# Kernel optimization log

Measured on AMD Instinct MI355X. Metric: run time of the kernel, lower is better.

Reference implementation:

```python
import jax, jax.numpy as jnp
import numpy as np

B, S = 16, 512
VD, TD, H, NH = 768, 768, 1024, 16
HD = H // NH
MAXREL = 128
THRESH = 2.0 / 3.0


def _bitlinear(x, W, b):
    # BitNet b1.58 eval-mode: ternary-quantize weights, rescale, dense matmul
    s = jnp.clip(jnp.mean(jnp.abs(W)), 1e-5, 1000.0)
    wn = jnp.clip(W / s, -10.0, 10.0)
    q = jnp.where(wn > THRESH, 1.0, jnp.where(wn < -THRESH, -1.0, 0.0))
    return x @ (q * s).T + b


def _ln(x, g, b, eps=1e-5):
    m = jnp.mean(x, axis=-1, keepdims=True)
    v = jnp.mean((x - m) ** 2, axis=-1, keepdims=True)
    return (x - m) * jax.lax.rsqrt(v + eps) * g + b


def setup_inputs() -> dict:
    key = jax.random.key(0)
    ks = jax.random.split(key, 10)
    def n(k, shape, std=0.02):
        return jax.random.normal(k, shape, dtype=jnp.float32) * std
    return dict(
        vision_features=jax.random.normal(ks[0], (B, VD), dtype=jnp.float32),
        text_features=jax.random.normal(ks[1], (B, S, TD), dtype=jnp.float32),
        W_vp=n(ks[2], (H, VD)), b_vp=jnp.zeros((H,), jnp.float32),
        W_tp=n(ks[3], (H, TD)), b_tp=jnp.zeros((H,), jnp.float32),
        W_tqkv=n(ks[4], (3 * H, H)), b_tqkv=jnp.zeros((3 * H,), jnp.float32),
        W_vout=n(ks[5], (H, H)), b_vout=jnp.zeros((H,), jnp.float32),
        W_tout=n(ks[6], (H, H)), b_tout=jnp.zeros((H,), jnp.float32),
        g_tn=jnp.ones((H,), jnp.float32), be_tn=jnp.zeros((H,), jnp.float32),
        g_i2t=jnp.ones((H,), jnp.float32), be_i2t=jnp.zeros((H,), jnp.float32),
        g_t2i=jnp.ones((H,), jnp.float32), be_t2i=jnp.zeros((H,), jnp.float32),
        alpha_i2t=jnp.zeros((1,), jnp.float32),
        alpha_t2i=jnp.zeros((1,), jnp.float32),
        rel_embed=n(ks[7], (2 * MAXREL + 1, NH)),
        text_mask=jnp.ones((B, S), dtype=bool),
    )


def reference(vision_features, text_features, W_vp, b_vp, W_tp, b_tp,
              W_tqkv, b_tqkv, W_vout, b_vout, W_tout, b_tout,
              g_tn, be_tn, g_i2t, be_i2t, g_t2i, be_t2i,
              alpha_i2t, alpha_t2i, rel_embed, text_mask):
    scale = HD ** -0.5
    vision_proj = _bitlinear(vision_features, W_vp, b_vp)            # [B,H]
    text_proj = _bitlinear(text_features, W_tp, b_tp)                # [B,S,H]

    # --- text self-attention with relative-position bias ---
    qkv = _bitlinear(_ln(text_proj, g_tn, be_tn), W_tqkv, b_tqkv)    # [B,S,3H]
    qkv = qkv.reshape(B, S, 3, NH, HD).transpose(2, 0, 3, 1, 4)      # [3,B,nh,S,hd]
    q, k, v = qkv[0], qkv[1], qkv[2]
    attn = jnp.einsum('bhqd,bhkd->bhqk', q, k) * scale
    coords = jnp.arange(S)
    rel = jnp.clip(coords[:, None] - coords[None, :], -MAXREL, MAXREL) + MAXREL
    attn = attn + rel_embed[rel].transpose(2, 0, 1)[None]            # +[1,nh,S,S]
    attn = jnp.where(text_mask[:, None, None, :], attn, -1e9)
    attn = jax.nn.softmax(attn, axis=-1)
    text_self = jnp.einsum('bhqk,bhkd->bhqd', attn, v)
    text_self = text_self.transpose(0, 2, 1, 3).reshape(B, S, H)
    text_self = text_proj + text_self                                # residual

    # --- image -> text cross-attention (vision token queries text) ---
    vq = jnp.broadcast_to(vision_proj[:, None], (B, S, H))
    vq = vq.reshape(B, S, NH, HD).transpose(0, 2, 1, 3)              # [B,nh,S,hd]
    tkv = text_self.reshape(B, S, NH, HD).transpose(0, 2, 1, 3)      # [B,nh,S,hd]
    i2t = jnp.einsum('bhqd,bhkd->bhqk', vq, tkv) * scale
    i2t = jnp.where(text_mask[:, None, None, :], i2t, -1e9)
    i2t = jax.nn.softmax(i2t, axis=-1)
    i2t_out = jnp.einsum('bhqk,bhkd->bhqd', i2t, tkv)
    i2t_out = i2t_out.transpose(0, 2, 1, 3).reshape(B, S, H).mean(axis=1)
    i2t_out = _ln(i2t_out, g_i2t, be_i2t)                            # [B,H]
    fused_vision = vision_proj + alpha_i2t * _bitlinear(i2t_out, W_vout, b_vout)

    # --- text -> image cross-attention (text queries single vision token) ---
    tq = text_self.reshape(B, S, NH, HD).transpose(0, 2, 1, 3)       # [B,nh,S,hd]
    vkv = vision_proj.reshape(B, 1, NH, HD).transpose(0, 2, 1, 3)    # [B,nh,1,hd]
    t2i = jnp.einsum('bhqd,bhkd->bhqk', tq, vkv) * scale             # [B,nh,S,1]
    t2i = jax.nn.softmax(t2i, axis=-1)
    t2i_out = jnp.einsum('bhqk,bhkd->bhqd', t2i, vkv)
    t2i_out = t2i_out.transpose(0, 2, 1, 3).reshape(B, S, H)
    t2i_out = _ln(t2i_out, g_t2i, be_t2i)
    fused_text = text_self + alpha_t2i * _bitlinear(t2i_out, W_tout, b_tout)

    return fused_vision, fused_text
```

## Files before the change

### kernel.cpp

```cpp
#include <hip/hip_runtime.h>
#include <cstdint>

#define B_   16
#define S_   512
#define VD_  768
#define TD_  768
#define H_   1024
#define NH_  16
#define HD_  64
#define H3_  3072

typedef __attribute__((ext_vector_type(8))) short bf16x8;
typedef __attribute__((ext_vector_type(4))) float f32x4;

__device__ __forceinline__ float b2f(unsigned short h) {
  union { unsigned u; float f; } x; x.u = ((unsigned)h) << 16; return x.f;
}
__device__ __forceinline__ unsigned short f2b(float f) {
  union { float f; unsigned u; } x; x.f = f;
  unsigned r = x.u + 0x7fffu + ((x.u >> 16) & 1u);
  return (unsigned short)(r >> 16);
}
__device__ __forceinline__ unsigned cvt_pk_bf16(float lo, float hi) {
  unsigned r;
  __asm__("v_cvt_pk_bf16_f32 %0, %1, %2" : "=v"(r) : "v"(lo), "v"(hi));
  return r;
}
__device__ __forceinline__ float fexp2(float x) {
#if __has_builtin(__builtin_amdgcn_exp2f)
  return __builtin_amdgcn_exp2f(x);
#else
  return exp2f(x);
#endif
}

__device__ __forceinline__ void gload_lds16(const void* g, void* lds) {
  __builtin_amdgcn_global_load_lds(
      (const __attribute__((address_space(1))) unsigned int*)g,
      (__attribute__((address_space(3))) unsigned int*)lds, 16, 0, 0);
}
__device__ __forceinline__ void lds_wave_fence() {
  __asm__ __volatile__("s_waitcnt lgkmcnt(0)" ::: "memory");
}

__global__ __launch_bounds__(256) void k_abssum_cvt(const float* __restrict__ w0, int n0,
                                                    const float* __restrict__ w1, int n1,
                                                    const float* __restrict__ w2, int n2,
                                                    const float* __restrict__ w3, int n3,
                                                    const float* __restrict__ w4, int n4,
                                                    double* __restrict__ partials,
                                                    const float* __restrict__ cvt_in,
                                                    unsigned short* __restrict__ cvt_out,
                                                    int cvt_n4) {
  int y = blockIdx.y;
  if (y == 5) {
    for (int i = blockIdx.x * 256 + threadIdx.x; i < cvt_n4; i += 128 * 256) {
      float4 v = ((const float4*)cvt_in)[i];
      ushort4 o; o.x = f2b(v.x); o.y = f2b(v.y); o.z = f2b(v.z); o.w = f2b(v.w);
      ((ushort4*)cvt_out)[i] = o;
    }
    return;
  }
  const float* w = y == 0 ? w0 : y == 1 ? w1 : y == 2 ? w2 : y == 3 ? w3 : w4;
  int n4q = (y == 0 ? n0 : y == 1 ? n1 : y == 2 ? n2 : y == 3 ? n3 : n4) >> 2;
  double s = 0.0;
  for (int i = blockIdx.x * 256 + threadIdx.x; i < n4q; i += 128 * 256) {
    float4 v = ((const float4*)w)[i];
    s += (double)fabsf(v.x) + (double)fabsf(v.y) + (double)fabsf(v.z) + (double)fabsf(v.w);
  }
#pragma unroll
  for (int off = 32; off > 0; off >>= 1) s += __shfl_down(s, off, 64);
  __shared__ double red[4];
  if ((threadIdx.x & 63) == 0) red[threadIdx.x >> 6] = s;
  __syncthreads();
  if (threadIdx.x == 0)
    partials[y * 128 + blockIdx.x] = red[0] + red[1] + red[2] + red[3];
}

__global__ __launch_bounds__(256) void k_quant5(const float* __restrict__ w0, int n0,
                                                const float* __restrict__ w1, int n1,
                                                const float* __restrict__ w2, int n2,
                                                const float* __restrict__ w3, int n3,
                                                const float* __restrict__ w4, int n4,
                                                unsigned short* __restrict__ q0,
                                                unsigned short* __restrict__ q1,
                                                unsigned short* __restrict__ q2,
                                                unsigned short* __restrict__ q3,
                                                unsigned short* __restrict__ q4,
                                                const double* __restrict__ partials,
                                                float* __restrict__ s_out) {
  int y = blockIdx.y;
  const float* w = y == 0 ? w0 : y == 1 ? w1 : y == 2 ? w2 : y == 3 ? w3 : w4;
  unsigned short* q = y == 0 ? q0 : y == 1 ? q1 : y == 2 ? q2 : y == 3 ? q3 : q4;
  int n = y == 0 ? n0 : y == 1 ? n1 : y == 2 ? n2 : y == 3 ? n3 : n4;
  const int t = threadIdx.x;
  __shared__ double sbc;
  if (t < 64) {
    double sv = partials[y * 128 + t] + partials[y * 128 + 64 + t];
#pragma unroll
    for (int off = 32; off > 0; off >>= 1) sv += __shfl_down(sv, off, 64);
    if (t == 0) sbc = sv;
  }
  __syncthreads();
  double s = fmin(fmax(sbc / (double)n, 1e-5), 1000.0);
  if (blockIdx.x == 0 && t == 0) s_out[y] = (float)s;
  int i = blockIdx.x * 256 + t;
  if (i < n) {
    double wn = (double)w[i] / s;
    unsigned short o = 0;
    if (wn > (2.0 / 3.0)) o = 0x3F80u;
    else if (wn < -(2.0 / 3.0)) o = 0xBF80u;
    q[i] = o;
  }
}

__global__ __launch_bounds__(256) void k_rowmat(const float* __restrict__ A,
                                                const unsigned short* __restrict__ W,
                                                const float* __restrict__ sptr,
                                                const float* __restrict__ bias,
                                                float* __restrict__ Cf,
                                                unsigned short* __restrict__ Cb,
                                                const float* __restrict__ resid,
                                                const float* __restrict__ alpha,
                                                int N, int K) {
  const int t = threadIdx.x, lane = t & 63;
  const int w_idx = blockIdx.x * 4 + (t >> 6);
  const int m = w_idx / N, n = w_idx - m * N;
  const int Kper = K >> 6;
  const float* a = A + (size_t)m * K + lane * Kper;
  const unsigned short* w = W + (size_t)n * K + lane * Kper;
  float acc = 0.f;
  for (int k = 0; k < Kper; k += 4) {
    float4 av = *(const float4*)(a + k);
    ushort4 wv = *(const ushort4*)(w + k);
    acc += av.x * b2f(wv.x) + av.y * b2f(wv.y) + av.z * b2f(wv.z) + av.w * b2f(wv.w);
  }
#pragma unroll
  for (int off = 32; off > 0; off >>= 1) acc += __shfl_down(acc, off, 64);
  if (lane == 0) {
    float v = acc * sptr[0] + bias[n];
    if (resid) v = resid[w_idx] + alpha[0] * v;
    Cf[w_idx] = v;
    if (Cb) Cb[w_idx] = f2b(v);
  }
}

__global__ __launch_bounds__(256) void k_ln(const float* __restrict__ x,
                                            const float* __restrict__ g,
                                            const float* __restrict__ be,
                                            float* __restrict__ of,
                                            unsigned short* __restrict__ ob) {
  int row = blockIdx.x, t = threadIdx.x;
  const float4* xr = (const float4*)(x + (size_t)row * H_);
  float4 v = xr[t];
  float s = v.x + v.y + v.z + v.w;
  float s2 = v.x * v.x + v.y * v.y + v.z * v.z + v.w * v.w;
#pragma unroll
  for (int off = 32; off > 0; off >>= 1) { s += __shfl_down(s, off, 64); s2 += __shfl_down(s2, off, 64); }
  __shared__ float rs[4], rs2[4];
  if ((t & 63) == 0) { rs[t >> 6] = s; rs2[t >> 6] = s2; }
  __syncthreads();
  s = rs[0] + rs[1] + rs[2] + rs[3];
  s2 = rs2[0] + rs2[1] + rs2[2] + rs2[3];
  float mean = s * (1.0f / H_);
  float var = s2 * (1.0f / H_) - mean * mean;
  float rstd = rsqrtf(var + 1e-5f);
  const float4 gv = ((const float4*)g)[t];
  const float4 bv = ((const float4*)be)[t];
  float4 o;
  o.x = (v.x - mean) * rstd * gv.x + bv.x;
  o.y = (v.y - mean) * rstd * gv.y + bv.y;
  o.z = (v.z - mean) * rstd * gv.z + bv.z;
  o.w = (v.w - mean) * rstd * gv.w + bv.w;
  if (of) ((float4*)(of + (size_t)row * H_))[t] = o;
  if (ob) {
    ushort4 ou; ou.x = f2b(o.x); ou.y = f2b(o.y); ou.z = f2b(o.z); ou.w = f2b(o.w);
    ((ushort4*)(ob + (size_t)row * H_))[t] = ou;
  }
}

template <int OUTB, int VT>
__global__ __launch_bounds__(256) void k_gemm(const unsigned short* __restrict__ A,
                                              const unsigned short* __restrict__ W,
                                              const float* __restrict__ sptr,
                                              const float* __restrict__ bias,
                                              float* __restrict__ Cf,
                                              unsigned short* __restrict__ Cb,
                                              unsigned short* __restrict__ vt,
                                              int M, int N, int K) {
  __shared__ __align__(16) unsigned short As[2][128 * 64];
  __shared__ __align__(16) unsigned short Bs[2][128 * 64];
  const int t = threadIdx.x, wave = t >> 6, lane = t & 63, quad = lane >> 4, l16 = lane & 15;
  const int bm = blockIdx.y * 128, bn = blockIdx.x * 128;
  const int wm = (wave >> 1) * 64, wn = (wave & 1) * 64;
  const int srow = lane >> 3, kc = (lane & 7) ^ srow;
  f32x4 acc[4][4];
#pragma unroll
  for (int i = 0; i < 4; ++i)
#pragma unroll
    for (int j = 0; j < 4; ++j) acc[i][j] = f32x4{0.f, 0.f, 0.f, 0.f};

  auto stage = [&](int kt, int buf) {
    const int k0 = kt * 64;
#pragma unroll
    for (int c = 0; c < 4; ++c) {
      int row = wave * 32 + c * 8 + srow;
      gload_lds16(A + (size_t)(bm + row) * K + k0 + kc * 8,
                  &As[buf][(wave * 32 + c * 8) * 64]);
      gload_lds16(W + (size_t)(bn + row) * K + k0 + kc * 8,
                  &Bs[buf][(wave * 32 + c * 8) * 64]);
    }
  };

  const int NT = K >> 6;
  stage(0, 0);
  for (int kt = 0; kt < NT; ++kt) {
    const int cur = kt & 1;
    if (kt + 1 < NT) {
      stage(kt + 1, cur ^ 1);
      __asm__ __volatile__("s_waitcnt vmcnt(8)" ::: "memory");
    } else {
      __asm__ __volatile__("s_waitcnt vmcnt(0)" ::: "memory");
    }
    __asm__ __volatile__("s_barrier" ::: "memory");
#pragma unroll
    for (int ks = 0; ks < 2; ++ks) {
      bf16x8 af[4], bfrg[4];
#pragma unroll
      for (int i = 0; i < 4; ++i) {
        int R = wm + i * 16 + l16;
        af[i] = *(const bf16x8*)&As[cur][R * 64 + (((ks * 4 + quad) ^ (R & 7)) * 8)];
      }
#pragma unroll
      for (int j = 0; j < 4; ++j) {
        int R = wn + j * 16 + l16;
        bfrg[j] = *(const bf16x8*)&Bs[cur][R * 64 + (((ks * 4 + quad) ^ (R & 7)) * 8)];
      }
      __builtin_amdgcn_s_setprio(1);
#pragma unroll
      for (int i = 0; i < 4; ++i)
#pragma unroll
        for (int j = 0; j < 4; ++j)
          acc[i][j] = __builtin_amdgcn_mfma_f32_16x16x32_bf16(af[i], bfrg[j], acc[i][j], 0, 0, 0);
      __builtin_amdgcn_s_setprio(0);
    }
    __asm__ __volatile__("s_barrier" ::: "memory");
  }
  float s = sptr[0];

  if (VT && bn >= 2 * H_) {
    unsigned short* T = (wave < 2) ? &As[0][wave * 1152] : &Bs[0][(wave - 2) * 1152];
    const int h = (bn + wn - 2 * H_) >> 6;
    const int b = (bm + wm) >> 9, s0 = (bm + wm) & (S_ - 1);
    const int chunk0 = lane * 2;
#pragma unroll
    for (int j = 0; j < 4; ++j) {
      int n = bn + wn + j * 16 + l16;
      float bv = bias[n];
#pragma unroll
      for (int i = 0; i < 4; ++i)
#pragma unroll
        for (int r = 0; r < 4; ++r)
          T[l16 * 72 + i * 16 + quad * 4 + r] = f2b(acc[i][j][r] * s + bv);
      lds_wave_fence();
#pragma unroll
      for (int cc = 0; cc < 2; ++cc) {
        int ch = chunk0 + cc, dr = ch >> 3, k8 = ch & 7;
        uint4 val = *(const uint4*)&T[dr * 72 + k8 * 8];
        *(uint4*)(vt + ((size_t)(b * NH_ + h) * HD_ + j * 16 + dr) * S_ + s0 + k8 * 8) = val;
      }
      lds_wave_fence();
    }
    return;
  }

#pragma unroll
  for (int j = 0; j < 4; ++j) {
    int n = bn + wn + j * 16 + l16;
    float bv = bias[n];
#pragma unroll
    for (int i = 0; i < 4; ++i) {
#pragma unroll
      for (int r = 0; r < 4; ++r) {
        int m = bm + wm + i * 16 + quad * 4 + r;
        float v = acc[i][j][r] * s + bv;
        if (OUTB) Cb[(size_t)m * N + n] = f2b(v);
        else      Cf[(size_t)m * N + n] = v;
      }
    }
  }
}

__global__ __launch_bounds__(512, 2) void k_flash(const unsigned short* __restrict__ qkv,
                                                  const unsigned short* __restrict__ vt,
                                                  const float* __restrict__ tp,
                                                  const float* __restrict__ rel,
                                                  const float* __restrict__ trow,
                                                  const float* __restrict__ a_t2i,
                                                  const unsigned short* __restrict__ vp_b,
                                                  float* __restrict__ out_text,
                                                  float* __restrict__ i2t_out) {
  const int h = blockIdx.x, b = blockIdx.y;
  __shared__ __align__(16) unsigned short Ks[2][64 * 64];
  __shared__ __align__(16) unsigned short Vs[2][64 * 64];
  __shared__ __align__(16) unsigned short Ps[8][16 * 72];
  __shared__ __align__(16) unsigned short TS[512][68];
  __shared__ float rels[257];
  __shared__ float qvs[64];
  __shared__ float scs[512];
  __shared__ float redm[8], redl[8];
  __shared__ float ored[8][64];
  const int t = threadIdx.x, wave = t >> 6, lane = t & 63, quad = lane >> 4, l16 = lane & 15;
  const int srow = lane >> 3;
  const int kcg = (lane & 7) ^ srow;
  const float LOG2E = 1.4426950408889634f;
  const float SC = 0.125f * LOG2E;

  for (int i = t; i < 257; i += 512) rels[i] = rel[i * NH_ + h] * LOG2E;
  if (t < 64) qvs[t] = b2f(vp_b[b * H_ + h * HD_ + t]);

  auto stage_kv = [&](int kt, int buf) {
    int row = wave * 8 + srow;
    gload_lds16(qkv + (size_t)(b * S_ + kt * 64 + row) * H3_ + H_ + h * HD_ + kcg * 8,
                &Ks[buf][(wave * 8) * 64]);
    gload_lds16(vt + ((size_t)(b * NH_ + h) * HD_ + row) * S_ + kt * 64 + kcg * 8,
                &Vs[buf][(wave * 8) * 64]);
  };
  auto stageQ = [&](int chunk, unsigned short* buf) {
    int row = chunk * 64 + wave * 8 + srow;
    gload_lds16(qkv + (size_t)(b * S_ + row) * H3_ + h * HD_ + kcg * 8,
                buf + (wave * 8) * 64);
  };

  bf16x8 aq0[4], aq1[4];
  unsigned short* qb0 = &Ks[0][0];
  unsigned short* qb1 = &Vs[0][0];
  unsigned short* qb2 = &Ks[1][0];
  unsigned short* qb3 = &Vs[1][0];
  stageQ(0, qb0); stageQ(1, qb1); stageQ(2, qb2); stageQ(3, qb3);
  __syncthreads();
  if (wave < 4) {
    const unsigned short* qb = wave == 0 ? qb0 : wave == 1 ? qb1 : wave == 2 ? qb2 : qb3;
#pragma unroll
    for (int rg = 0; rg < 4; ++rg) {
      int R = rg * 16 + l16;
      aq0[rg] = *(const bf16x8*)&qb[R * 64 + ((quad ^ (R & 7)) * 8)];
      aq1[rg] = *(const bf16x8*)&qb[R * 64 + (((4 + quad) ^ (R & 7)) * 8)];
    }
  }
  __syncthreads();
  stageQ(4, qb0); stageQ(5, qb1); stageQ(6, qb2); stageQ(7, qb3);
  __syncthreads();
  if (wave >= 4) {
    const int c = wave - 4;
    const unsigned short* qb = c == 0 ? qb0 : c == 1 ? qb1 : c == 2 ? qb2 : qb3;
#pragma unroll
    for (int rg = 0; rg < 4; ++rg) {
      int R = rg * 16 + l16;
      aq0[rg] = *(const bf16x8*)&qb[R * 64 + ((quad ^ (R & 7)) * 8)];
      aq1[rg] = *(const bf16x8*)&qb[R * 64 + (((4 + quad) ^ (R & 7)) * 8)];
    }
  }
  __syncthreads();
  stage_kv(0, 0);

  float mrun[4], lrun[4];
  f32x4 o[4][4];
#pragma unroll
  for (int rg = 0; rg < 4; ++rg) {
    mrun[rg] = -1e30f; lrun[rg] = 0.f;
#pragma unroll
    for (int j = 0; j < 4; ++j) o[rg][j] = f32x4{0.f, 0.f, 0.f, 0.f};
  }

  for (int kt = 0; kt < 8; ++kt) {
    const int cur = kt & 1;
    __syncthreads();
    if (kt < 7) stage_kv(kt + 1, cur ^ 1);

#pragma unroll
    for (int rg = 0; rg < 4; ++rg) {
      const int qb_row = wave * 64 + rg * 16;
      const int dqb = qb_row - kt * 64;
      const bool uni = (dqb >= 192) || (dqb <= -144);
      const float bu = uni ? rels[dqb >= 192 ? 256 : 0] : 0.f;
      const int qg = qb_row + l16;

      float pv[4][4];
#pragma unroll
      for (int j = 0; j < 4; ++j) {
        int R = j * 16 + l16;
        bf16x8 kb0 = *(const bf16x8*)&Ks[cur][R * 64 + ((quad ^ (R & 7)) * 8)];
        bf16x8 kb1 = *(const bf16x8*)&Ks[cur][R * 64 + (((4 + quad) ^ (R & 7)) * 8)];
        f32x4 z = f32x4{0.f, 0.f, 0.f, 0.f};
        z = __builtin_amdgcn_mfma_f32_16x16x32_bf16(kb0, aq0[rg], z, 0, 0, 0);
        z = __builtin_amdgcn_mfma_f32_16x16x32_bf16(kb1, aq1[rg], z, 0, 0, 0);
        if (uni) {
#pragma unroll
          for (int r = 0; r < 4; ++r) pv[j][r] = z[r] * SC + bu;
        } else {
          const int kg0 = kt * 64 + j * 16 + quad * 4;
#pragma unroll
          for (int r = 0; r < 4; ++r) {
            int rix = min(max(qg - kg0 - r, -128), 128) + 128;
            pv[j][r] = z[r] * SC + rels[rix];
          }
        }
      }
      float x = pv[0][0];
#pragma unroll
      for (int j = 0; j < 4; ++j)
#pragma unroll
        for (int r = 0; r < 4; ++r) x = fmaxf(x, pv[j][r]);
      x = fmaxf(x, __shfl_xor(x, 16, 64));
      x = fmaxf(x, __shfl_xor(x, 32, 64));
      if (!__all(x <= mrun[rg])) {
        float mn = fmaxf(mrun[rg], x);
        float al = fexp2(mrun[rg] - mn);
        mrun[rg] = mn;
        lrun[rg] *= al;
        float al0 = __shfl(al, quad * 4 + 0, 64);
        float al1 = __shfl(al, quad * 4 + 1, 64);
        float al2 = __shfl(al, quad * 4 + 2, 64);
        float al3 = __shfl(al, quad * 4 + 3, 64);
#pragma unroll
        for (int jd = 0; jd < 4; ++jd) {
          o[rg][jd][0] *= al0; o[rg][jd][1] *= al1;
          o[rg][jd][2] *= al2; o[rg][jd][3] *= al3;
        }
      }
      float rsum = 0.f;
#pragma unroll
      for (int j = 0; j < 4; ++j)
#pragma unroll
        for (int r = 0; r < 4; ++r) {
          float p = fexp2(pv[j][r] - mrun[rg]);
          pv[j][r] = p;
          rsum += p;
        }
      rsum += __shfl_xor(rsum, 16, 64);
      rsum += __shfl_xor(rsum, 32, 64);
      lrun[rg] += rsum;
      unsigned char* psb = (unsigned char*)&Ps[wave][0] + l16 * 144 + quad * 8;
#pragma unroll
      for (int j = 0; j < 4; ++j) {
        uint2 pk;
        pk.x = cvt_pk_bf16(pv[j][0], pv[j][1]);
        pk.y = cvt_pk_bf16(pv[j][2], pv[j][3]);
        *(uint2*)(psb + j * 32) = pk;
      }
      lds_wave_fence();
#pragma unroll
      for (int ks = 0; ks < 2; ++ks) {
        bf16x8 ap = *(const bf16x8*)&Ps[wave][l16 * 72 + ks * 32 + quad * 8];
#pragma unroll
        for (int jd = 0; jd < 4; ++jd) {
          int R = jd * 16 + l16;
          int C = ks * 4 + quad;
          bf16x8 vb = *(const bf16x8*)&Vs[cur][R * 64 + ((C ^ (R & 7)) * 8)];
          o[rg][jd] = __builtin_amdgcn_mfma_f32_16x16x32_bf16(ap, vb, o[rg][jd], 0, 0, 0);
        }
      }
      lds_wave_fence();
    }
  }
  float a2 = a_t2i[0];
#pragma unroll
  for (int rg = 0; rg < 4; ++rg) {
    float il[4];
#pragma unroll
    for (int r = 0; r < 4; ++r) {
      float lr = __shfl(lrun[rg], quad * 4 + r, 64);
      il[r] = 1.0f / lr;
    }
#pragma unroll
    for (int jd = 0; jd < 4; ++jd) {
#pragma unroll
      for (int r = 0; r < 4; ++r) {
        int sl = wave * 64 + rg * 16 + quad * 4 + r;
        int g = b * S_ + sl;
        int col = h * HD_ + jd * 16 + l16;
        float ov = o[rg][jd][r] * il[r];
        float ts = tp[(size_t)g * H_ + col] + ov;
        TS[sl][jd * 16 + l16] = f2b(ts);
        out_text[(size_t)g * H_ + col] = ts + a2 * trow[b * H_ + col];
      }
    }
  }
  __syncthreads();

  const int grp = t >> 6, d = t & 63;
  float a = 0.f;
#pragma unroll
  for (int dc = 0; dc < 16; ++dc) {
    uint2 u = *(const uint2*)&TS[t][dc * 4];
    const unsigned short* p = (const unsigned short*)&u;
    a += qvs[dc * 4 + 0] * b2f(p[0]) + qvs[dc * 4 + 1] * b2f(p[1])
       + qvs[dc * 4 + 2] * b2f(p[2]) + qvs[dc * 4 + 3] * b2f(p[3]);
  }
  float sc0 = a * 0.125f;
  float m = sc0;
#pragma unroll
  for (int off = 1; off < 64; off <<= 1) m = fmaxf(m, __shfl_xor(m, off, 64));
  if (lane == 0) redm[wave] = m;
  __syncthreads();
  m = redm[0];
#pragma unroll
  for (int wv = 1; wv < 8; ++wv) m = fmaxf(m, redm[wv]);
  float p = __expf(sc0 - m);
  scs[t] = p;
  float ls = p;
#pragma unroll
  for (int off = 1; off < 64; off <<= 1) ls += __shfl_xor(ls, off, 64);
  if (lane == 0) redl[wave] = ls;
  __syncthreads();
  float tot = redl[0] + redl[1] + redl[2] + redl[3] + redl[4] + redl[5] + redl[6] + redl[7];
  float acc = 0.f;
  for (int k = grp; k < 512; k += 8)
    acc += scs[k] * b2f(TS[k][d]);
  ored[grp][d] = acc;
  __syncthreads();
  if (t < 64) {
    float o8 = ored[0][t] + ored[1][t] + ored[2][t] + ored[3][t]
             + ored[4][t] + ored[5][t] + ored[6][t] + ored[7][t];
    i2t_out[b * H_ + h * HD_ + t] = o8 / tot;
  }
}

extern "C" void kernel_launch(void* const* d_in, const int* in_sizes, int n_in,
                              void* d_out, int out_size, void* d_ws, size_t ws_size,
                              hipStream_t stream) {
  const float* vf     = (const float*)d_in[0];
  const float* tf     = (const float*)d_in[1];
  const float* W_vp   = (const float*)d_in[2];
  const float* b_vp   = (const float*)d_in[3];
  const float* W_tp   = (const float*)d_in[4];
  const float* b_tp   = (const float*)d_in[5];
  const float* W_tqkv = (const float*)d_in[6];
  const float* b_tqkv = (const float*)d_in[7];
  const float* W_vout = (const float*)d_in[8];
  const float* b_vout = (const float*)d_in[9];
  const float* W_tout = (const float*)d_in[10];
  const float* b_tout = (const float*)d_in[11];
  const float* g_tn   = (const float*)d_in[12];
  const float* be_tn  = (const float*)d_in[13];
  const float* g_i2t  = (const float*)d_in[14];
  const float* be_i2t = (const float*)d_in[15];
  const float* g_t2i  = (const float*)d_in[16];
  const float* be_t2i = (const float*)d_in[17];
  const float* a_i2t  = (const float*)d_in[18];
  const float* a_t2i  = (const float*)d_in[19];
  const float* rel    = (const float*)d_in[20];

  size_t off = 0;
  auto alloc = [&](size_t bytes) -> void* {
    void* p = (char*)d_ws + off;
    off += (bytes + 255) & ~(size_t)255;
    return p;
  };
  double* partials = (double*)alloc(5 * 128 * 8);
  float* scales    = (float*)alloc(64);
  unsigned short* q_vp   = (unsigned short*)alloc((size_t)H_ * VD_ * 2);
  unsigned short* q_tp   = (unsigned short*)alloc((size_t)H_ * TD_ * 2);
  unsigned short* q_tqkv = (unsigned short*)alloc((size_t)H3_ * H_ * 2);
  unsigned short* q_vout = (unsigned short*)alloc((size_t)H_ * H_ * 2);
  unsigned short* q_tout = (unsigned short*)alloc((size_t)H_ * H_ * 2);
  unsigned short* tf_b   = (unsigned short*)alloc((size_t)B_ * S_ * TD_ * 2);
  float* text_proj       = (float*)alloc((size_t)B_ * S_ * H_ * 4);
  unsigned short* ln_tp  = (unsigned short*)alloc((size_t)B_ * S_ * H_ * 2);
  unsigned short* qkv    = (unsigned short*)alloc((size_t)B_ * S_ * H3_ * 2);
  unsigned short* vt     = (unsigned short*)alloc((size_t)B_ * NH_ * HD_ * S_ * 2);
  float* vision_proj     = (float*)alloc((size_t)B_ * H_ * 4);
  unsigned short* vp_b   = (unsigned short*)alloc((size_t)B_ * H_ * 2);
  float* ln_t2i_f        = (float*)alloc((size_t)B_ * H_ * 4);
  float* trow            = (float*)alloc((size_t)B_ * H_ * 4);
  float* i2t_out         = (float*)alloc((size_t)B_ * H_ * 4);
  float* ln_i2t_f        = (float*)alloc((size_t)B_ * H_ * 4);

  float* out_vision = (float*)d_out;
  float* out_text   = (float*)d_out + B_ * H_;

  k_abssum_cvt<<<dim3(128, 6), 256, 0, stream>>>(W_vp, H_ * VD_, W_tp, H_ * TD_,
                                                 W_tqkv, H3_ * H_, W_vout, H_ * H_,
                                                 W_tout, H_ * H_, partials,
                                                 tf, tf_b, B_ * S_ * TD_ / 4);
  k_quant5<<<dim3((H3_ * H_ + 255) / 256, 5), 256, 0, stream>>>(
      W_vp, H_ * VD_, W_tp, H_ * TD_, W_tqkv, H3_ * H_, W_vout, H_ * H_, W_tout, H_ * H_,
      q_vp, q_tp, q_tqkv, q_vout, q_tout, partials, scales);

  k_rowmat<<<(B_ * H_) / 4, 256, 0, stream>>>(vf, q_vp, scales + 0, b_vp,
                                              vision_proj, vp_b, nullptr, nullptr, H_, VD_);
  k_ln<<<B_, 256, 0, stream>>>(vision_proj, g_t2i, be_t2i, ln_t2i_f, nullptr);
  k_rowmat<<<(B_ * H_) / 4, 256, 0, stream>>>(ln_t2i_f, q_tout, scales + 4, b_tout,
                                              trow, nullptr, nullptr, nullptr, H_, H_);

  k_gemm<0, 0><<<dim3(H_ / 128, (B_ * S_) / 128), 256, 0, stream>>>(
      tf_b, q_tp, scales + 1, b_tp, text_proj, nullptr, nullptr, B_ * S_, H_, TD_);
  k_ln<<<B_ * S_, 256, 0, stream>>>(text_proj, g_tn, be_tn, nullptr, ln_tp);
  k_gemm<1, 1><<<dim3(H3_ / 128, (B_ * S_) / 128), 256, 0, stream>>>(
      ln_tp, q_tqkv, scales + 2, b_tqkv, nullptr, qkv, vt, B_ * S_, H3_, H_);
  k_flash<<<dim3(NH_, B_), 512, 0, stream>>>(qkv, vt, text_proj, rel, trow, a_t2i,
                                             vp_b, out_text, i2t_out);
  k_ln<<<B_, 256, 0, stream>>>(i2t_out, g_i2t, be_i2t, ln_i2t_f, nullptr);
  k_rowmat<<<(B_ * H_) / 4, 256, 0, stream>>>(ln_i2t_f, q_vout, scales + 3, b_vout,
                                              out_vision, nullptr, vision_proj, a_i2t, H_, H_);
}
```

Measured before the change: 358.5 us.

## Fuse LayerNorm into row matvec kernels and swizzle GEMM block order

Adds a k_rowmat_ln kernel that computes the row LayerNorm in shared memory and then does the ternary-weight matvec, replacing two separate k_ln + k_rowmat launches and their intermediate buffers. It also remaps GEMM block indices into groups of 4 rows by 2 column halves to improve L2 reuse of A and W tiles. The fused kernel recomputes the LayerNorm in every block, and the swizzle changes the order in which tiles are scheduled.

```diff
diff --git a/kernel.cpp b/kernel.cpp
--- a/kernel.cpp
+++ b/kernel.cpp
@@ -145,6 +145,61 @@
   }
 }
 
+__global__ __launch_bounds__(256) void k_rowmat_ln(const float* __restrict__ X,
+                                                   const float* __restrict__ g,
+                                                   const float* __restrict__ be,
+                                                   const unsigned short* __restrict__ W,
+                                                   const float* __restrict__ sptr,
+                                                   const float* __restrict__ bias,
+                                                   float* __restrict__ Cf,
+                                                   const float* __restrict__ resid,
+                                                   const float* __restrict__ alpha,
+                                                   int N) {
+  const int t = threadIdx.x, lane = t & 63;
+  const int w_idx = blockIdx.x * 4 + (t >> 6);
+  const int m = (blockIdx.x * 4) / N;
+  const int n = w_idx - m * N;
+  __shared__ float xln[H_];
+  __shared__ float rs[4], rs2[4];
+  float4 v = ((const float4*)(X + (size_t)m * H_))[t];
+  float s = v.x + v.y + v.z + v.w;
+  float s2 = v.x * v.x + v.y * v.y + v.z * v.z + v.w * v.w;
+#pragma unroll
+  for (int off = 32; off > 0; off >>= 1) { s += __shfl_down(s, off, 64); s2 += __shfl_down(s2, off, 64); }
+  if ((t & 63) == 0) { rs[t >> 6] = s; rs2[t >> 6] = s2; }
+  __syncthreads();
+  s = rs[0] + rs[1] + rs[2] + rs[3];
+  s2 = rs2[0] + rs2[1] + rs2[2] + rs2[3];
+  float mean = s * (1.0f / H_);
+  float var = s2 * (1.0f / H_) - mean * mean;
+  float rstd = rsqrtf(var + 1e-5f);
+  const float4 gv = ((const float4*)g)[t];
+  const float4 bv = ((const float4*)be)[t];
+  float4 o;
+  o.x = (v.x - mean) * rstd * gv.x + bv.x;
+  o.y = (v.y - mean) * rstd * gv.y + bv.y;
+  o.z = (v.z - mean) * rstd * gv.z + bv.z;
+  o.w = (v.w - mean) * rstd * gv.w + bv.w;
+  ((float4*)xln)[t] = o;
+  __syncthreads();
+  const float* a = xln + lane * 16;
+  const unsigned short* w = W + (size_t)n * H_ + lane * 16;
+  float acc = 0.f;
+#pragma unroll
+  for (int k = 0; k < 16; k += 4) {
+    float4 av = *(const float4*)(a + k);
+    ushort4 wv = *(const ushort4*)(w + k);
+    acc += av.x * b2f(wv.x) + av.y * b2f(wv.y) + av.z * b2f(wv.z) + av.w * b2f(wv.w);
+  }
+#pragma unroll
+  for (int off = 32; off > 0; off >>= 1) acc += __shfl_down(acc, off, 64);
+  if (lane == 0) {
+    float vv = acc * sptr[0] + bias[n];
+    if (resid) vv = resid[w_idx] + alpha[0] * vv;
+    Cf[w_idx] = vv;
+  }
+}
+
 __global__ __launch_bounds__(256) void k_ln(const float* __restrict__ x,
                                             const float* __restrict__ g,
                                             const float* __restrict__ be,
@@ -191,7 +246,18 @@
   __shared__ __align__(16) unsigned short As[2][128 * 64];
   __shared__ __align__(16) unsigned short Bs[2][128 * 64];
   const int t = threadIdx.x, wave = t >> 6, lane = t & 63, quad = lane >> 4, l16 = lane & 15;
-  const int bm = blockIdx.y * 128, bn = blockIdx.x * 128;
+  int bxs = blockIdx.x, bys = blockIdx.y;
+  {
+    const int GX = gridDim.x, GY = gridDim.y;
+    if ((GX & 1) == 0 && (GY & 3) == 0) {
+      int ell = bys * GX + bxs;
+      int xx = ell & 7, r = ell >> 3;
+      int hx = GX >> 1;
+      bxs = (xx >> 2) * hx + r % hx;
+      bys = (r / hx) * 4 + (xx & 3);
+    }
+  }
+  const int bm = bys * 128, bn = bxs * 128;
   const int wm = (wave >> 1) * 64, wn = (wave & 1) * 64;
   const int srow = lane >> 3, kc = (lane & 7) ^ srow;
   f32x4 acc[4][4];
@@ -572,10 +638,8 @@
   unsigned short* vt     = (unsigned short*)alloc((size_t)B_ * NH_ * HD_ * S_ * 2);
   float* vision_proj     = (float*)alloc((size_t)B_ * H_ * 4);
   unsigned short* vp_b   = (unsigned short*)alloc((size_t)B_ * H_ * 2);
-  float* ln_t2i_f        = (float*)alloc((size_t)B_ * H_ * 4);
   float* trow            = (float*)alloc((size_t)B_ * H_ * 4);
   float* i2t_out         = (float*)alloc((size_t)B_ * H_ * 4);
-  float* ln_i2t_f        = (float*)alloc((size_t)B_ * H_ * 4);
 
   float* out_vision = (float*)d_out;
   float* out_text   = (float*)d_out + B_ * H_;
@@ -590,9 +654,9 @@
 
   k_rowmat<<<(B_ * H_) / 4, 256, 0, stream>>>(vf, q_vp, scales + 0, b_vp,
                                               vision_proj, vp_b, nullptr, nullptr, H_, VD_);
-  k_ln<<<B_, 256, 0, stream>>>(vision_proj, g_t2i, be_t2i, ln_t2i_f, nullptr);
-  k_rowmat<<<(B_ * H_) / 4, 256, 0, stream>>>(ln_t2i_f, q_tout, scales + 4, b_tout,
-                                              trow, nullptr, nullptr, nullptr, H_, H_);
+  k_rowmat_ln<<<(B_ * H_) / 4, 256, 0, stream>>>(vision_proj, g_t2i, be_t2i, q_tout,
+                                                 scales + 4, b_tout, trow,
+                                                 nullptr, nullptr, H_);
 
   k_gemm<0, 0><<<dim3(H_ / 128, (B_ * S_) / 128), 256, 0, stream>>>(
       tf_b, q_tp, scales + 1, b_tp, text_proj, nullptr, nullptr, B_ * S_, H_, TD_);
@@ -601,7 +665,7 @@
       ln_tp, q_tqkv, scales + 2, b_tqkv, nullptr, qkv, vt, B_ * S_, H3_, H_);
   k_flash<<<dim3(NH_, B_), 512, 0, stream>>>(qkv, vt, text_proj, rel, trow, a_t2i,
                                              vp_b, out_text, i2t_out);
-  k_ln<<<B_, 256, 0, stream>>>(i2t_out, g_i2t, be_i2t, ln_i2t_f, nullptr);
-  k_rowmat<<<(B_ * H_) / 4, 256, 0, stream>>>(ln_i2t_f, q_vout, scales + 3, b_vout,
-                                              out_vision, nullptr, vision_proj, a_i2t, H_, H_);
-}
+  k_rowmat_ln<<<(B_ * H_) / 4, 256, 0, stream>>>(i2t_out, g_i2t, be_i2t, q_vout,
+                                                 scales + 3, b_vout, out_vision,
+                                                 vision_proj, a_i2t, H_);
+}
```

Result: faster. 350.6 us (-2.2%).
